# Kernel optimization log

Hardware: AMD Instinct MI355X
Metric: run time of the kernel (lower is better)

Reference implementation:

```python
import jax, jax.numpy as jnp
import numpy as np

FP8_MAX = 448.0  # torch.finfo(torch.float8_e4m3fn).max

def per_tensor_quantize(t):
    amax = jnp.max(jnp.abs(t))
    scale = FP8_MAX / jnp.maximum(amax, 1e-12)
    q = jnp.clip(t * scale, -FP8_MAX, FP8_MAX).astype(jnp.float8_e4m3fn)
    return q, (1.0 / scale).astype(jnp.float32)

def fp8_gemm(q, a_scale, w_q, w_scale, out_dtype):
    # emulate: linear(A.to(out)*a_scale, B.to(out)*b_scale)
    A = q.astype(out_dtype) * a_scale
    B = w_q.astype(out_dtype) * w_scale
    return A @ B.T

def setup_inputs() -> dict:
    key = jax.random.key(0)
    k1, k2, k3, k4 = jax.random.split(key, 4)
    tokens, hidden, ffn = 4096, 4096, 10752
    return {
        "x": jax.random.normal(k1, (tokens, hidden), jnp.float32),
        "expert_w1": jax.random.normal(k2, (ffn, hidden), jnp.float32) * 0.02,
        "expert_v1": jax.random.normal(k3, (ffn, hidden), jnp.float32) * 0.02,
        "expert_w2": jax.random.normal(k4, (ffn, hidden), jnp.float32) * 0.02,
    }

def reference(x, expert_w1, expert_v1, expert_w2):
    dt = x.dtype
    # weight quantization (as done in _quantize_weights per expert)
    w1_q, w1_s = per_tensor_quantize(expert_w1)
    v1_q, v1_s = per_tensor_quantize(expert_v1)
    w2_q, w2_s = per_tensor_quantize(expert_w2)
    # activation quantization + gate/up GEMMs
    qin, x_s = per_tensor_quantize(x)
    gate = fp8_gemm(qin, x_s, w1_q, w1_s, dt)          # [N, ffn]
    up = fp8_gemm(qin, x_s, v1_q, v1_s, dt)            # [N, ffn]
    inter = jax.nn.silu(gate) * up                      # fused GLU
    qmid, m_s = per_tensor_quantize(inter)
    # down proj uses expert_w2.t() -> B = [hidden, ffn]
    down = fp8_gemm(qmid, m_s, w2_q.T, w2_s, dt)        # [N, hidden]
    return down
```

## Files before the change

kernel.cpp:

```cpp
#include <hip/hip_runtime.h>
#include <cstdint>
#include <cstddef>

typedef float f32x4 __attribute__((ext_vector_type(4)));
typedef float f32x16 __attribute__((ext_vector_type(16)));
typedef int i32x4 __attribute__((ext_vector_type(4)));
typedef int i32x8 __attribute__((ext_vector_type(8)));
typedef unsigned char u8;
typedef unsigned short u16;
typedef u16 u16x8 __attribute__((ext_vector_type(8)));
typedef unsigned int u32;
typedef u32 u32x4 __attribute__((ext_vector_type(4)));

static __device__ __forceinline__ void gload_lds16(const void* g, void* l) {
  __builtin_amdgcn_global_load_lds(
      (__attribute__((address_space(1))) void*)(void*)g,
      (__attribute__((address_space(3))) void*)l,
      16, 0, 0);
}

#if defined(__has_builtin)
#if __has_builtin(__builtin_amdgcn_cvt_pk_fp8_f32)
#define HAVE_HW_FP8 1
#endif
#endif

__device__ __forceinline__ u8 f32_to_e4m3_sw(float x) {
  unsigned s = (__float_as_uint(x) >> 24) & 0x80;
  float ax = fabsf(x);
  if (!(ax > 0.0f)) return (u8)s;
  if (ax >= 448.0f) return (u8)(s | 0x7e);
  if (ax < 0.015625f) {
    int m = (int)rintf(ax * 512.0f);
    if (m >= 8) return (u8)(s | 0x08);
    return (u8)(s | m);
  }
  int e = ilogbf(ax);
  int m = (int)rintf(ldexpf(ax, 3 - e));
  if (m == 16) { ++e; m = 8; }
  return (u8)(s | ((e + 7) << 3) | (m - 8));
}

__device__ __forceinline__ unsigned cvt4_fp8(float a, float b, float c, float d) {
#ifdef HAVE_HW_FP8
  int lo = __builtin_amdgcn_cvt_pk_fp8_f32(a, b, 0, false);
  return (unsigned)__builtin_amdgcn_cvt_pk_fp8_f32(c, d, lo, true);
#else
  return (unsigned)f32_to_e4m3_sw(a) | ((unsigned)f32_to_e4m3_sw(b) << 8) |
         ((unsigned)f32_to_e4m3_sw(c) << 16) | ((unsigned)f32_to_e4m3_sw(d) << 24);
#endif
}

__device__ __forceinline__ float clamp448(float x) {
  return fminf(fmaxf(x, -448.f), 448.f);
}

__device__ __forceinline__ u16 f32_to_bf16(float x) {
  unsigned u = __float_as_uint(x);
  return (u16)((u + 0x7FFFu + ((u >> 16) & 1u)) >> 16);
}

__global__ __launch_bounds__(256) void amax_kernel(const float* __restrict__ src, size_t n4,
                                                   unsigned* __restrict__ out) {
  float m = 0.0f;
  size_t stride = (size_t)gridDim.x * blockDim.x;
  const f32x4* p = (const f32x4*)src;
  for (size_t i = (size_t)blockIdx.x * blockDim.x + threadIdx.x; i < n4; i += stride) {
    f32x4 v = p[i];
    m = fmaxf(m, fmaxf(fmaxf(fabsf(v[0]), fabsf(v[1])), fmaxf(fabsf(v[2]), fabsf(v[3]))));
  }
#pragma unroll
  for (int off = 32; off > 0; off >>= 1) m = fmaxf(m, __shfl_down(m, off));
  __shared__ float red[4];
  int lane = threadIdx.x & 63, wid = threadIdx.x >> 6;
  if (lane == 0) red[wid] = m;
  __syncthreads();
  if (threadIdx.x == 0) {
    float v = fmaxf(fmaxf(red[0], red[1]), fmaxf(red[2], red[3]));
    atomicMax(out, __float_as_uint(v));
  }
}

__global__ __launch_bounds__(256) void quant_kernel(const float* __restrict__ src,
                                                    u8* __restrict__ dst,
                                                    const unsigned* __restrict__ amax_bits,
                                                    size_t n8) {
  float amax = __uint_as_float(*amax_bits);
  float scale = 448.0f / fmaxf(amax, 1e-12f);
  size_t stride = (size_t)gridDim.x * blockDim.x;
  const f32x4* p = (const f32x4*)src;
  uint2* q = (uint2*)dst;
  for (size_t i = (size_t)blockIdx.x * blockDim.x + threadIdx.x; i < n8; i += stride) {
    f32x4 a = p[2 * i], b = p[2 * i + 1];
    uint2 r;
    r.x = cvt4_fp8(clamp448(a[0] * scale), clamp448(a[1] * scale),
                   clamp448(a[2] * scale), clamp448(a[3] * scale));
    r.y = cvt4_fp8(clamp448(b[0] * scale), clamp448(b[1] * scale),
                   clamp448(b[2] * scale), clamp448(b[3] * scale));
    q[i] = r;
  }
}

__global__ __launch_bounds__(256) void pack_f32_kernel(const float* __restrict__ src,
                                                       u8* __restrict__ dst,
                                                       const unsigned* __restrict__ amax_bits,
                                                       int K) {
  float amax = __uint_as_float(*amax_bits);
  float scale = 448.0f / fmaxf(amax, 1e-12f);
  int c = (int)blockIdx.x * 256 + (int)threadIdx.x;
  int m = c & 4095;
  int kb = c >> 12;
  const f32x4* s = (const f32x4*)(src + (size_t)m * K + kb * 32);
  unsigned w[8];
#pragma unroll
  for (int j = 0; j < 8; ++j) {
    f32x4 v = s[j];
    w[j] = cvt4_fp8(clamp448(v[0] * scale), clamp448(v[1] * scale),
                    clamp448(v[2] * scale), clamp448(v[3] * scale));
  }
  u32x4* d = (u32x4*)(dst + ((size_t)kb * 4096 + m) * 32);
  d[0] = u32x4{w[0], w[1], w[2], w[3]};
  d[1] = u32x4{w[4], w[5], w[6], w[7]};
}

__global__ __launch_bounds__(256) void pack_bf16_kernel(const u16* __restrict__ src,
                                                        u8* __restrict__ dst,
                                                        const unsigned* __restrict__ amax_bits,
                                                        int K) {
  float amax = __uint_as_float(*amax_bits);
  float scale = 448.0f / fmaxf(amax, 1e-12f);
  int c = (int)blockIdx.x * 256 + (int)threadIdx.x;
  int m = c & 4095;
  int kb = c >> 12;
  const u16x8* s = (const u16x8*)(src + (size_t)m * K + kb * 32);
  unsigned w[8];
#pragma unroll
  for (int j = 0; j < 4; ++j) {
    u16x8 v = s[j];
    float f0 = __uint_as_float((unsigned)v[0] << 16) * scale;
    float f1 = __uint_as_float((unsigned)v[1] << 16) * scale;
    float f2 = __uint_as_float((unsigned)v[2] << 16) * scale;
    float f3 = __uint_as_float((unsigned)v[3] << 16) * scale;
    float f4 = __uint_as_float((unsigned)v[4] << 16) * scale;
    float f5 = __uint_as_float((unsigned)v[5] << 16) * scale;
    float f6 = __uint_as_float((unsigned)v[6] << 16) * scale;
    float f7 = __uint_as_float((unsigned)v[7] << 16) * scale;
    w[2 * j]     = cvt4_fp8(clamp448(f0), clamp448(f1), clamp448(f2), clamp448(f3));
    w[2 * j + 1] = cvt4_fp8(clamp448(f4), clamp448(f5), clamp448(f6), clamp448(f7));
  }
  u32x4* d = (u32x4*)(dst + ((size_t)kb * 4096 + m) * 32);
  d[0] = u32x4{w[0], w[1], w[2], w[3]};
  d[1] = u32x4{w[4], w[5], w[6], w[7]};
}

__global__ __launch_bounds__(256) void quantT_kernel(const float* __restrict__ src,
                                                     u8* __restrict__ dst,
                                                     const unsigned* __restrict__ amax_bits,
                                                     int R, int C) {
  __shared__ float t[64][65];
  float amax = __uint_as_float(*amax_bits);
  float scale = 448.0f / fmaxf(amax, 1e-12f);
  int nbr = R >> 6;
  int br = (int)blockIdx.x % nbr, bc = (int)blockIdx.x / nbr;
  int r0 = br * 64, c0 = bc * 64;
  int tid = threadIdx.x;
  int lc = tid & 63, lr = tid >> 6;
#pragma unroll
  for (int i = 0; i < 16; ++i)
    t[lr + i * 4][lc] = src[(size_t)(r0 + lr + i * 4) * C + c0 + lc];
  __syncthreads();
  int qd = tid & 15, xbase = tid >> 4;
#pragma unroll
  for (int i = 0; i < 4; ++i) {
    int x = xbase + 16 * i;
    float v0 = clamp448(t[4 * qd + 0][x] * scale);
    float v1 = clamp448(t[4 * qd + 1][x] * scale);
    float v2 = clamp448(t[4 * qd + 2][x] * scale);
    float v3 = clamp448(t[4 * qd + 3][x] * scale);
    *(unsigned*)(dst + (size_t)(c0 + x) * R + r0 + 4 * qd) = cvt4_fp8(v0, v1, v2, v3);
  }
}

__device__ __forceinline__ int swz_key(int r) { return (r >> 2) & 3; }

__device__ __forceinline__ int swz_off32(int r, int h) {
  return r * 64 + ((((h << 1) ^ swz_key(r)) << 4));
}

__device__ __forceinline__ i32x8 ld_frag(const u8* base, int r, int h) {
  int o = swz_off32(r, h);
  i32x8 f;
  f.lo = *(const i32x4*)(base + o);
  f.hi = *(const i32x4*)(base + (o ^ 16));
  return f;
}

__device__ __forceinline__ i32x8 ld_a_g(const u8* p) {
  i32x8 f;
  f.lo = *(const i32x4*)p;
  f.hi = *(const i32x4*)(p + 16);
  return f;
}

#define MFMA_MX(a, b, c) \
  __builtin_amdgcn_mfma_scale_f32_32x32x64_f8f6f4((a), (b), (c), 0, 0, 0, 0x7F7F7F7F, 0, 0x7F7F7F7F)

__global__ __launch_bounds__(256, 2) void gemm1_gateup(
    const u8* __restrict__ Apk, const u8* __restrict__ Wq, const u8* __restrict__ Vq,
    const unsigned* __restrict__ scal, u16* __restrict__ inter,
    unsigned* __restrict__ amax_mid, int M, int N, int K) {
  __shared__ __align__(16) u8 lW[3][8192], lV[3][8192];
  __shared__ float red[4];
  int tid = threadIdx.x;
  int lane = tid & 63, wid = tid >> 6;
  int wm = wid >> 1, wn = wid & 1;

  int bid = (int)blockIdx.x;
  int bm = bid & 31;
  int bn = bid >> 5;

  int r0 = tid >> 2;
  int kblk = ((tid & 3) ^ swz_key(r0)) << 4;
  const u8* wS = Wq + (size_t)(bn * 128 + r0) * K + kblk;
  const u8* vS = Vq + (size_t)(bn * 128 + r0) * K + kblk;
  size_t rK = (size_t)64 * K;

  f32x16 g00 = (f32x16)(0.f), g01 = (f32x16)(0.f), g10 = (f32x16)(0.f), g11 = (f32x16)(0.f);
  f32x16 u00 = (f32x16)(0.f), u01 = (f32x16)(0.f), u10 = (f32x16)(0.f), u11 = (f32x16)(0.f);

  int rfrag = lane & 31;
  int h = lane >> 5;
  int arow = wm * 64 + rfrag;
  int brow = wn * 64 + rfrag;

  const size_t tStride = (size_t)64 * M;
  const u8* aP = Apk + 32 * ((size_t)M * h + (size_t)(bm * 128 + arow));

  int NT = K >> 6;
  {
    gload_lds16(wS + 0, lW[0] + tid * 16);
    gload_lds16(wS + 0 + rK, lW[0] + 4096 + tid * 16);
    gload_lds16(vS + 0, lV[0] + tid * 16);
    gload_lds16(vS + 0 + rK, lV[0] + 4096 + tid * 16);
    gload_lds16(wS + 64, lW[1] + tid * 16);
    gload_lds16(wS + 64 + rK, lW[1] + 4096 + tid * 16);
    gload_lds16(vS + 64, lV[1] + tid * 16);
    gload_lds16(vS + 64 + rK, lV[1] + 4096 + tid * 16);
  }
  i32x8 ac0 = ld_a_g(aP);
  i32x8 ac1 = ld_a_g(aP + 1024);
  i32x8 an0 = ac0, an1 = ac1;

  for (int t = 0; t < NT; ++t) {
    int cur = t % 3;
    int nx = cur + 2; if (nx >= 3) nx -= 3;
    int kt2 = (t + 2) * 64;
    bool do_stage = (t + 2) < NT;
    bool do_pref = (t + 1) < NT;
    if (do_pref) {
      asm volatile("s_waitcnt vmcnt(8)" ::: "memory");
    } else {
      asm volatile("s_waitcnt vmcnt(0)" ::: "memory");
    }
    __builtin_amdgcn_s_barrier();
    i32x8 w0 = ld_frag(lW[cur], brow, h);
    i32x8 w1 = ld_frag(lW[cur], brow + 32, h);
    if (do_pref) {
      const u8* ap = aP + (size_t)(t + 1) * tStride;
      an0 = ld_a_g(ap);
      an1 = ld_a_g(ap + 1024);
    }
    if (do_stage) {
      gload_lds16(wS + kt2, lW[nx] + tid * 16);
      gload_lds16(wS + kt2 + rK, lW[nx] + 4096 + tid * 16);
    }
    __builtin_amdgcn_s_barrier();
    __builtin_amdgcn_s_setprio(1);
    g00 = MFMA_MX(ac0, w0, g00);
    g10 = MFMA_MX(ac1, w0, g10);
    g01 = MFMA_MX(ac0, w1, g01);
    g11 = MFMA_MX(ac1, w1, g11);
    __builtin_amdgcn_s_setprio(0);
    __builtin_amdgcn_s_barrier();
    i32x8 v0 = ld_frag(lV[cur], brow, h);
    i32x8 v1 = ld_frag(lV[cur], brow + 32, h);
    if (do_stage) {
      gload_lds16(vS + kt2, lV[nx] + tid * 16);
      gload_lds16(vS + kt2 + rK, lV[nx] + 4096 + tid * 16);
    }
    __builtin_amdgcn_s_barrier();
    __builtin_amdgcn_s_setprio(1);
    u00 = MFMA_MX(ac0, v0, u00);
    u10 = MFMA_MX(ac1, v0, u10);
    u01 = MFMA_MX(ac0, v1, u01);
    u11 = MFMA_MX(ac1, v1, u11);
    __builtin_amdgcn_s_setprio(0);
    ac0 = an0; ac1 = an1;
  }

  float ax = __uint_as_float(scal[0]);
  float aw = __uint_as_float(scal[1]);
  float av = __uint_as_float(scal[2]);
  float inv_x = 1.0f / (448.0f / fmaxf(ax, 1e-12f));
  float inv_w = 1.0f / (448.0f / fmaxf(aw, 1e-12f));
  float inv_v = 1.0f / (448.0f / fmaxf(av, 1e-12f));
  float sg = inv_x * inv_w, su = inv_x * inv_v;

  int rb = bm * 128 + wm * 64 + h * 4;
  int cb = bn * 128 + wn * 64 + rfrag;
  float lmax = 0.0f;
#pragma unroll
  for (int mi = 0; mi < 2; ++mi)
#pragma unroll
    for (int ni = 0; ni < 2; ++ni) {
      const f32x16& gg = mi ? (ni ? g11 : g10) : (ni ? g01 : g00);
      const f32x16& uu = mi ? (ni ? u11 : u10) : (ni ? u01 : u00);
#pragma unroll
      for (int q = 0; q < 16; ++q) {
        int rr = rb + mi * 32 + (q & 3) + 8 * (q >> 2);
        float gv = gg[q] * sg;
        float uv = uu[q] * su;
        float iv = gv / (1.0f + expf(-gv)) * uv;
        inter[(size_t)rr * N + (cb + ni * 32)] = f32_to_bf16(iv);
        lmax = fmaxf(lmax, fabsf(iv));
      }
    }
#pragma unroll
  for (int off = 32; off > 0; off >>= 1) lmax = fmaxf(lmax, __shfl_down(lmax, off));
  if (lane == 0) red[wid] = lmax;
  __syncthreads();
  if (tid == 0)
    atomicMax(amax_mid, __float_as_uint(fmaxf(fmaxf(red[0], red[1]), fmaxf(red[2], red[3]))));
}

__global__ __launch_bounds__(256, 2) void gemm2_down(
    const u8* __restrict__ Apk, const u8* __restrict__ Bq,
    const unsigned* __restrict__ amax_a, const unsigned* __restrict__ amax_b,
    float* __restrict__ out, int M, int N, int K) {
  __shared__ __align__(16) u8 lB[3][8192];
  int tid = threadIdx.x;
  int lane = tid & 63, wid = tid >> 6;
  int wm = wid >> 1, wn = wid & 1;

  int bid = (int)blockIdx.x;
  int bm = bid & 31;
  int bn = bid >> 5;

  int r0 = tid >> 2;
  int kblk = ((tid & 3) ^ swz_key(r0)) << 4;
  const u8* bS = Bq + (size_t)(bn * 128 + r0) * K + kblk;
  size_t rK = (size_t)64 * K;

  f32x16 c00 = (f32x16)(0.f), c01 = (f32x16)(0.f);
  f32x16 c10 = (f32x16)(0.f), c11 = (f32x16)(0.f);

  int rfrag = lane & 31;
  int h = lane >> 5;
  int arow = wm * 64 + rfrag;
  int brow = wn * 64 + rfrag;

  const size_t tStride = (size_t)64 * M;
  const u8* aP = Apk + 32 * ((size_t)M * h + (size_t)(bm * 128 + arow));

  int NT = K >> 6;
  {
    gload_lds16(bS + 0, lB[0] + tid * 16);
    gload_lds16(bS + 0 + rK, lB[0] + 4096 + tid * 16);
    gload_lds16(bS + 64, lB[1] + tid * 16);
    gload_lds16(bS + 64 + rK, lB[1] + 4096 + tid * 16);
  }
  i32x8 ac0 = ld_a_g(aP);
  i32x8 ac1 = ld_a_g(aP + 1024);
  i32x8 an0 = ac0, an1 = ac1;

  for (int t = 0; t < NT; ++t) {
    int cur = t % 3;
    int nx = cur + 2; if (nx >= 3) nx -= 3;
    int kt2 = (t + 2) * 64;
    bool do_stage = (t + 2) < NT;
    bool do_pref = (t + 1) < NT;
    if (do_pref) {
      asm volatile("s_waitcnt vmcnt(6)" ::: "memory");
    } else {
      asm volatile("s_waitcnt vmcnt(0)" ::: "memory");
    }
    __builtin_amdgcn_s_barrier();
    i32x8 b0 = ld_frag(lB[cur], brow, h);
    if (do_pref) {
      const u8* ap = aP + (size_t)(t + 1) * tStride;
      an0 = ld_a_g(ap);
      an1 = ld_a_g(ap + 1024);
    }
    if (do_stage) {
      gload_lds16(bS + kt2, lB[nx] + tid * 16);
      gload_lds16(bS + kt2 + rK, lB[nx] + 4096 + tid * 16);
    }
    __builtin_amdgcn_s_barrier();
    __builtin_amdgcn_s_setprio(1);
    c00 = MFMA_MX(ac0, b0, c00);
    c10 = MFMA_MX(ac1, b0, c10);
    __builtin_amdgcn_s_setprio(0);
    __builtin_amdgcn_s_barrier();
    i32x8 b1 = ld_frag(lB[cur], brow + 32, h);
    __builtin_amdgcn_s_barrier();
    __builtin_amdgcn_s_setprio(1);
    c01 = MFMA_MX(ac0, b1, c01);
    c11 = MFMA_MX(ac1, b1, c11);
    __builtin_amdgcn_s_setprio(0);
    ac0 = an0; ac1 = an1;
  }

  float sa = 1.0f / (448.0f / fmaxf(__uint_as_float(*amax_a), 1e-12f));
  float sb = 1.0f / (448.0f / fmaxf(__uint_as_float(*amax_b), 1e-12f));
  float sc = sa * sb;

  int rb = bm * 128 + wm * 64 + h * 4;
  int cb = bn * 128 + wn * 64 + rfrag;
#pragma unroll
  for (int mi = 0; mi < 2; ++mi)
#pragma unroll
    for (int ni = 0; ni < 2; ++ni) {
      const f32x16& cc = mi ? (ni ? c11 : c10) : (ni ? c01 : c00);
#pragma unroll
      for (int q = 0; q < 16; ++q) {
        int rr = rb + mi * 32 + (q & 3) + 8 * (q >> 2);
        out[(size_t)rr * N + (cb + ni * 32)] = cc[q] * sc;
      }
    }
}

extern "C" void kernel_launch(void* const* d_in, const int* in_sizes, int n_in,
                              void* d_out, int out_size, void* d_ws, size_t ws_size,
                              hipStream_t stream) {
  const float* x  = (const float*)d_in[0];
  const float* w1 = (const float*)d_in[1];
  const float* v1 = (const float*)d_in[2];
  const float* w2 = (const float*)d_in[3];
  const int M = 4096, H = 4096, F = 10752;

  u8* ws = (u8*)d_ws;
  unsigned* scal = (unsigned*)ws;
  u8* xpk  = ws + 256;
  u8* w1q  = xpk  + (size_t)M * H;
  u8* v1q  = w1q  + (size_t)F * H;
  u8* w2qT = v1q  + (size_t)F * H;
  u8* midpk = w2qT + (size_t)F * H;
  u16* inter = (u16*)(midpk + (size_t)M * F);

  hipMemsetAsync(scal, 0, 256, stream);
  amax_kernel<<<2048, 256, 0, stream>>>(x,  (size_t)M * H / 4, scal + 0);
  amax_kernel<<<2048, 256, 0, stream>>>(w1, (size_t)F * H / 4, scal + 1);
  amax_kernel<<<2048, 256, 0, stream>>>(v1, (size_t)F * H / 4, scal + 2);
  amax_kernel<<<2048, 256, 0, stream>>>(w2, (size_t)F * H / 4, scal + 3);

  pack_f32_kernel<<<(M * (H / 32)) / 256, 256, 0, stream>>>(x, xpk, scal + 0, H);
  quant_kernel<<<2048, 256, 0, stream>>>(w1, w1q, scal + 1, (size_t)F * H / 8);
  quant_kernel<<<2048, 256, 0, stream>>>(v1, v1q, scal + 2, (size_t)F * H / 8);
  quantT_kernel<<<(F / 64) * (H / 64), 256, 0, stream>>>(w2, w2qT, scal + 3, F, H);

  gemm1_gateup<<<(M / 128) * (F / 128), 256, 0, stream>>>(xpk, w1q, v1q, scal, inter,
                                                          scal + 4, M, F, H);
  pack_bf16_kernel<<<(M * (F / 32)) / 256, 256, 0, stream>>>(inter, midpk, scal + 4, F);
  gemm2_down<<<(M / 128) * (H / 128), 256, 0, stream>>>(midpk, w2qT, scal + 4, scal + 3,
                                                        (float*)d_out, M, H, F);
}
```

Measured before the change: 988.9 us.

## Batch amax/quant launches and merge LDS fragment loads to cut GEMM barriers

Replaces the four amax launches with one kernel that splits its 2048 blocks across x, w1, v1 and w2, and merges the two w1/v1 quant launches into one. Inside both GEMM main loops, all B/W/V fragment loads and LDS staging are hoisted into the first phase, which removes one barrier pair per K-step. This cuts launch overhead and per-iteration synchronisation, at the cost of more live fragment registers and larger bursts of outstanding loads. The unchanged vmcnt waits may now count differently because more loads are issued before them.

New measurement: 975.4 us. About the same (-1.4%).

```diff
diff --git a/kernel.cpp b/kernel.cpp
--- a/kernel.cpp
+++ b/kernel.cpp
@@ -60,12 +60,24 @@
   return (u16)((u + 0x7FFFu + ((u >> 16) & 1u)) >> 16);
 }
 
-__global__ __launch_bounds__(256) void amax_kernel(const float* __restrict__ src, size_t n4,
-                                                   unsigned* __restrict__ out) {
+__global__ __launch_bounds__(256) void amax4_kernel(const float* __restrict__ x,
+                                                    const float* __restrict__ w1,
+                                                    const float* __restrict__ v1,
+                                                    const float* __restrict__ w2,
+                                                    unsigned* __restrict__ out) {
+  const size_t nX = (size_t)4096 * 4096 / 4;
+  const size_t nW = (size_t)10752 * 4096 / 4;
+  int b = (int)blockIdx.x;
+  const f32x4* p;
+  size_t n4;
+  int slot, b0, nb;
+  if (b < 232)       { p = (const f32x4*)x;  n4 = nX; slot = 0; b0 = 0;    nb = 232; }
+  else if (b < 840)  { p = (const f32x4*)w1; n4 = nW; slot = 1; b0 = 232;  nb = 608; }
+  else if (b < 1448) { p = (const f32x4*)v1; n4 = nW; slot = 2; b0 = 840;  nb = 608; }
+  else               { p = (const f32x4*)w2; n4 = nW; slot = 3; b0 = 1448; nb = 600; }
   float m = 0.0f;
-  size_t stride = (size_t)gridDim.x * blockDim.x;
-  const f32x4* p = (const f32x4*)src;
-  for (size_t i = (size_t)blockIdx.x * blockDim.x + threadIdx.x; i < n4; i += stride) {
+  size_t stride = (size_t)nb * 256;
+  for (size_t i = (size_t)(b - b0) * 256 + threadIdx.x; i < n4; i += stride) {
     f32x4 v = p[i];
     m = fmaxf(m, fmaxf(fmaxf(fabsf(v[0]), fabsf(v[1])), fmaxf(fabsf(v[2]), fabsf(v[3]))));
   }
@@ -77,26 +89,32 @@
   __syncthreads();
   if (threadIdx.x == 0) {
     float v = fmaxf(fmaxf(red[0], red[1]), fmaxf(red[2], red[3]));
-    atomicMax(out, __float_as_uint(v));
-  }
-}
-
-__global__ __launch_bounds__(256) void quant_kernel(const float* __restrict__ src,
-                                                    u8* __restrict__ dst,
-                                                    const unsigned* __restrict__ amax_bits,
-                                                    size_t n8) {
-  float amax = __uint_as_float(*amax_bits);
+    atomicMax(out + slot, __float_as_uint(v));
+  }
+}
+
+__global__ __launch_bounds__(256) void quant2_kernel(const float* __restrict__ w1,
+                                                     u8* __restrict__ w1q,
+                                                     const float* __restrict__ v1,
+                                                     u8* __restrict__ v1q,
+                                                     const unsigned* __restrict__ scal,
+                                                     size_t n8) {
+  int b = (int)blockIdx.x;
+  const f32x4* p;
+  uint2* q;
+  float amax;
+  int rb;
+  if (b < 1024) { p = (const f32x4*)w1; q = (uint2*)w1q; amax = __uint_as_float(scal[1]); rb = b; }
+  else          { p = (const f32x4*)v1; q = (uint2*)v1q; amax = __uint_as_float(scal[2]); rb = b - 1024; }
   float scale = 448.0f / fmaxf(amax, 1e-12f);
-  size_t stride = (size_t)gridDim.x * blockDim.x;
-  const f32x4* p = (const f32x4*)src;
-  uint2* q = (uint2*)dst;
-  for (size_t i = (size_t)blockIdx.x * blockDim.x + threadIdx.x; i < n8; i += stride) {
-    f32x4 a = p[2 * i], b = p[2 * i + 1];
+  size_t stride = (size_t)1024 * 256;
+  for (size_t i = (size_t)rb * 256 + threadIdx.x; i < n8; i += stride) {
+    f32x4 a = p[2 * i], c = p[2 * i + 1];
     uint2 r;
     r.x = cvt4_fp8(clamp448(a[0] * scale), clamp448(a[1] * scale),
                    clamp448(a[2] * scale), clamp448(a[3] * scale));
-    r.y = cvt4_fp8(clamp448(b[0] * scale), clamp448(b[1] * scale),
-                   clamp448(b[2] * scale), clamp448(b[3] * scale));
+    r.y = cvt4_fp8(clamp448(c[0] * scale), clamp448(c[1] * scale),
+                   clamp448(c[2] * scale), clamp448(c[3] * scale));
     q[i] = r;
   }
 }
@@ -265,6 +283,8 @@
     __builtin_amdgcn_s_barrier();
     i32x8 w0 = ld_frag(lW[cur], brow, h);
     i32x8 w1 = ld_frag(lW[cur], brow + 32, h);
+    i32x8 v0 = ld_frag(lV[cur], brow, h);
+    i32x8 v1 = ld_frag(lV[cur], brow + 32, h);
     if (do_pref) {
       const u8* ap = aP + (size_t)(t + 1) * tStride;
       an0 = ld_a_g(ap);
@@ -273,6 +293,8 @@
     if (do_stage) {
       gload_lds16(wS + kt2, lW[nx] + tid * 16);
       gload_lds16(wS + kt2 + rK, lW[nx] + 4096 + tid * 16);
+      gload_lds16(vS + kt2, lV[nx] + tid * 16);
+      gload_lds16(vS + kt2 + rK, lV[nx] + 4096 + tid * 16);
     }
     __builtin_amdgcn_s_barrier();
     __builtin_amdgcn_s_setprio(1);
@@ -280,16 +302,6 @@
     g10 = MFMA_MX(ac1, w0, g10);
     g01 = MFMA_MX(ac0, w1, g01);
     g11 = MFMA_MX(ac1, w1, g11);
-    __builtin_amdgcn_s_setprio(0);
-    __builtin_amdgcn_s_barrier();
-    i32x8 v0 = ld_frag(lV[cur], brow, h);
-    i32x8 v1 = ld_frag(lV[cur], brow + 32, h);
-    if (do_stage) {
-      gload_lds16(vS + kt2, lV[nx] + tid * 16);
-      gload_lds16(vS + kt2 + rK, lV[nx] + 4096 + tid * 16);
-    }
-    __builtin_amdgcn_s_barrier();
-    __builtin_amdgcn_s_setprio(1);
     u00 = MFMA_MX(ac0, v0, u00);
     u10 = MFMA_MX(ac1, v0, u10);
     u01 = MFMA_MX(ac0, v1, u01);
@@ -386,6 +398,7 @@
     }
     __builtin_amdgcn_s_barrier();
     i32x8 b0 = ld_frag(lB[cur], brow, h);
+    i32x8 b1 = ld_frag(lB[cur], brow + 32, h);
     if (do_pref) {
       const u8* ap = aP + (size_t)(t + 1) * tStride;
       an0 = ld_a_g(ap);
@@ -399,11 +412,6 @@
     __builtin_amdgcn_s_setprio(1);
     c00 = MFMA_MX(ac0, b0, c00);
     c10 = MFMA_MX(ac1, b0, c10);
-    __builtin_amdgcn_s_setprio(0);
-    __builtin_amdgcn_s_barrier();
-    i32x8 b1 = ld_frag(lB[cur], brow + 32, h);
-    __builtin_amdgcn_s_barrier();
-    __builtin_amdgcn_s_setprio(1);
     c01 = MFMA_MX(ac0, b1, c01);
     c11 = MFMA_MX(ac1, b1, c11);
     __builtin_amdgcn_s_setprio(0);
@@ -448,14 +456,10 @@
   u16* inter = (u16*)(midpk + (size_t)M * F);
 
   hipMemsetAsync(scal, 0, 256, stream);
-  amax_kernel<<<2048, 256, 0, stream>>>(x,  (size_t)M * H / 4, scal + 0);
-  amax_kernel<<<2048, 256, 0, stream>>>(w1, (size_t)F * H / 4, scal + 1);
-  amax_kernel<<<2048, 256, 0, stream>>>(v1, (size_t)F * H / 4, scal + 2);
-  amax_kernel<<<2048, 256, 0, stream>>>(w2, (size_t)F * H / 4, scal + 3);
+  amax4_kernel<<<2048, 256, 0, stream>>>(x, w1, v1, w2, scal);
 
   pack_f32_kernel<<<(M * (H / 32)) / 256, 256, 0, stream>>>(x, xpk, scal + 0, H);
-  quant_kernel<<<2048, 256, 0, stream>>>(w1, w1q, scal + 1, (size_t)F * H / 8);
-  quant_kernel<<<2048, 256, 0, stream>>>(v1, v1q, scal + 2, (size_t)F * H / 8);
+  quant2_kernel<<<2048, 256, 0, stream>>>(w1, w1q, v1, v1q, scal, (size_t)F * H / 8);
   quantT_kernel<<<(F / 64) * (H / 64), 256, 0, stream>>>(w2, w2qT, scal + 3, F, H);
 
   gemm1_gateup<<<(M / 128) * (F / 128), 256, 0, stream>>>(xpk, w1q, v1q, scal, inter,
```
